# Performance work log

Measured on AMD Instinct MI355X. Metric: run time of the kernel, lower is better.

Reference implementation:

```python
import jax, jax.numpy as jnp
import numpy as np

B, T, M, D = 2, 2048, 2048, 128
H = M // D
ROTARY_BASE = 10000
NORM_EPS = 1e-6
QK_SCALE = 1.0 / D  # mult = sqrt(qk_scale) applied to both q and k
INFTY_APPROX = 1e30


def setup_inputs() -> dict:
    key = jax.random.key(0)
    ks = jax.random.split(key, 6)
    w_scale = M ** (-0.5)
    return {
        "x": jax.random.normal(ks[0], (B, T, M), jnp.float32),
        "wq": jax.random.normal(ks[1], (M, H, D), jnp.float32) * w_scale,
        "wk": jax.random.normal(ks[2], (M, H, D), jnp.float32) * w_scale,
        "wv": jax.random.normal(ks[3], (M, H, D), jnp.float32) * w_scale,
        "wo": jax.random.normal(ks[4], (H, D, M), jnp.float32) * w_scale,
        "gq": jnp.zeros((H, 1, D), jnp.float32),
        "bq": jnp.zeros((H, 1, D), jnp.float32),
        "gk": jnp.zeros((H, 1, D), jnp.float32),
        "bk": jnp.zeros((H, 1, D), jnp.float32),
    }


def _qk_layernorm(x, g, b):
    # x: [B,H,T,D]; g,b: [H,1,D]; centered RMS norm with trainable (1+g), b
    x = x - jnp.mean(x, axis=-1, keepdims=True)
    x = x / jnp.sqrt(jnp.mean(jnp.square(x), axis=-1, keepdims=True) + NORM_EPS)
    return x * (1.0 + g)[None] + b[None]


def _rotary(x):
    # x: [B,H,T,D]; half-split rotary encoding
    half = D // 2
    positions = jnp.arange(T, dtype=jnp.float32)[:, None]          # [T,1]
    ang_freqs = jnp.power(float(ROTARY_BASE), -jnp.arange(half, dtype=jnp.float32) / half)[None, :]  # [1,half]
    radians = positions * ang_freqs                                  # [T,half]
    cos = jnp.cos(radians)[None, None].astype(x.dtype)               # [1,1,T,half]
    sin = jnp.sin(radians)[None, None].astype(x.dtype)
    even, odd = jnp.split(x, 2, axis=-1)
    return jnp.concatenate([even * cos - odd * sin, even * sin + odd * cos], axis=-1)


def reference(x, wq, wk, wv, wo, gq, bq, gk, bk):
    q = jnp.einsum('bim,mhd->bhid', x, wq)
    k = jnp.einsum('bim,mhd->bhid', x, wk)
    v = jnp.einsum('bim,mhd->bhid', x, wv)
    q = _rotary(_qk_layernorm(q, gq, bq))
    k = _rotary(_qk_layernorm(k, gk, bk))
    mult = jnp.asarray(QK_SCALE ** 0.5, dtype=x.dtype)
    s = jnp.einsum('bhid,bhjd->bhij', q * mult, k * mult)            # [B,H,T,T]
    i = jnp.arange(T)[:, None]
    j = jnp.arange(T)[None, :]
    future = (i < j)[None, None]                                      # mask future positions
    s = s - jnp.asarray(INFTY_APPROX, dtype=s.dtype) * future
    p = jax.nn.softmax(s, axis=-1)
    o = jnp.einsum('bhij,bhjd->bhid', p, v)
    return jnp.einsum('bhid,hdm->bim', o, wo)
```

## Files before the change

### kernel.cpp

```cpp
#include <hip/hip_runtime.h>


#define NB 2
#define NT 2048
#define NM 2048
#define NH 16
#define ND 128

typedef __attribute__((ext_vector_type(4))) float f32x4;
typedef __attribute__((ext_vector_type(8))) short bf16x8;
typedef __attribute__((ext_vector_type(4))) short bf16x4;

#define AS1 __attribute__((address_space(1)))
#define AS3 __attribute__((address_space(3)))

__device__ __forceinline__ unsigned short f2bf(float f){
  unsigned int u = __float_as_uint(f);
  u = (u + 0x7fffu + ((u >> 16) & 1u)) >> 16;
  return (unsigned short)u;
}
__device__ __forceinline__ float bf2f(short s){
  return __uint_as_float(((unsigned int)(unsigned short)s) << 16);
}
__device__ __forceinline__ float wredsum(float v){
  #pragma unroll
  for (int m = 1; m < 64; m <<= 1) v += __shfl_xor(v, m);
  return v;
}
__device__ __forceinline__ void gload_lds16(const void* g, void* l){
  __builtin_amdgcn_global_load_lds((const AS1 void*)g, (AS3 void*)l, 16, 0, 0);
}

__global__ __launch_bounds__(64) void rope_table_k(float* ctab, float* stab){
  int t = blockIdx.x, i = threadIdx.x;
  float freq = __expf(-(float)i * (9.210340371976184f / 64.0f));
  float ang = (float)t * freq;
  ctab[t * 64 + i] = cosf(ang);
  stab[t * 64 + i] = sinf(ang);
}

__global__ __launch_bounds__(256) void cast_x_k(const float* __restrict__ x,
                                                short* __restrict__ xb){
  size_t gid = (size_t)blockIdx.x * 256 + threadIdx.x;
  float4 v = *(const float4*)(x + gid * 4);
  bf16x4 o;
  o[0] = (short)f2bf(v.x); o[1] = (short)f2bf(v.y);
  o[2] = (short)f2bf(v.z); o[3] = (short)f2bf(v.w);
  *(bf16x4*)(xb + gid * 4) = o;
}

__global__ __launch_bounds__(256) void transpose_w_k(const float* __restrict__ wq,
                                                     const float* __restrict__ wk,
                                                     const float* __restrict__ wv,
                                                     const float* __restrict__ wo,
                                                     short* __restrict__ wT){
  __shared__ float tl[32][33];
  int z = blockIdx.z;
  const float* src = (z == 0) ? wq : (z == 1) ? wk : (z == 2) ? wv : wo;
  short* dst = wT + (size_t)z * 2048 * 2048;
  int n0 = blockIdx.x * 32, k0 = blockIdx.y * 32;
  int cx = threadIdx.x & 31, ry = threadIdx.x >> 5;
  #pragma unroll
  for (int p = 0; p < 4; ++p)
    tl[ry + 8 * p][cx] = src[(size_t)(k0 + ry + 8 * p) * 2048 + n0 + cx];
  __syncthreads();
  #pragma unroll
  for (int p = 0; p < 4; ++p)
    dst[(size_t)(n0 + ry + 8 * p) * 2048 + k0 + cx] =
        (short)f2bf(tl[cx][ry + 8 * p]);
}

#define NKT 32
__global__ __launch_bounds__(512, 2) void gemm256_k(const short* __restrict__ A,
                                                    const short* __restrict__ Bt,
                                                    short* __restrict__ Cq){
  extern __shared__ char lds[];
  const int tid = threadIdx.x;
  const int wid = tid >> 6, lane = tid & 63;
  const int lrow = lane & 15, g8 = lane >> 4;
  const int wm = wid >> 2, wn = wid & 3;
  const int Kdim = 2048;

  int bid = blockIdx.x;
  int s = (bid & 7) * 48 + (bid >> 3);
  const int bx = s & 15;
  const int by = s >> 4;
  const int m0 = bx * 256, n0 = by * 256;

  const int r8 = lane >> 3;
  const int gcol = ((lane & 7) ^ r8) * 8;
  const short* Ab = A  + (size_t)(m0 + wid * 8 + r8) * Kdim + gcol;
  const short* Bb = Bt + (size_t)(n0 + wid * 8 + r8) * Kdim + gcol;

  f32x4 acc[8][4] = {};

  auto STAGE = [&](int c, int kt){
    #pragma unroll
    for (int h = 0; h < 2; ++h)
      #pragma unroll
      for (int l = 0; l < 2; ++l){
        size_t roff = (size_t)(h * 128 + l * 64) * Kdim + kt * 64;
        char* la = lds + c * 32768 + h * 16384 + l * 8192 + wid * 1024;
        gload_lds16(Ab + roff, la);
        gload_lds16(Bb + roff, la + 65536);
      }
  };
  auto ldA = [&](int c, int mi, int kk) -> bf16x8 {
    int row = mi * 16 + lrow;
    int col = (kk * 64 + g8 * 16) ^ ((lrow & 7) << 4);
    return *(const bf16x8*)(lds + c * 32768 + wm * 16384 + row * 128 + col);
  };
  auto ldB = [&](int c, int ni, int kk) -> bf16x8 {
    int row = (wn & 1) * 64 + ni * 16 + lrow;
    int col = (kk * 64 + g8 * 16) ^ ((lrow & 7) << 4);
    return *(const bf16x8*)(lds + 65536 + c * 32768 + (wn >> 1) * 16384 + row * 128 + col);
  };

  STAGE(0, 0);

  for (int kt = 0; kt < NKT; ++kt){
    const int c = kt & 1;
    asm volatile("s_waitcnt vmcnt(0)" ::: "memory");
    __builtin_amdgcn_s_barrier();
    if (kt + 1 < NKT) STAGE(c ^ 1, kt + 1);

    #pragma unroll
    for (int kk = 0; kk < 2; ++kk){
      bf16x8 bfr[4];
      #pragma unroll
      for (int ni = 0; ni < 4; ++ni) bfr[ni] = ldB(c, ni, kk);
      #pragma unroll
      for (int mh = 0; mh < 2; ++mh){
        bf16x8 afr[4];
        #pragma unroll
        for (int mi = 0; mi < 4; ++mi) afr[mi] = ldA(c, mh * 4 + mi, kk);
        #pragma unroll
        for (int mi = 0; mi < 4; ++mi)
          #pragma unroll
          for (int ni = 0; ni < 4; ++ni)
            acc[mh * 4 + mi][ni] = __builtin_amdgcn_mfma_f32_16x16x32_bf16(
                afr[mi], bfr[ni], acc[mh * 4 + mi][ni], 0, 0, 0);
      }
    }
  }

  #pragma unroll
  for (int mi = 0; mi < 8; ++mi){
    int rowb = m0 + wm * 128 + mi * 16 + g8 * 4;
    #pragma unroll
    for (int ni = 0; ni < 4; ++ni){
      int col = n0 + wn * 64 + ni * 16 + lrow;
      int tsel = col >> 11;
      int hd = col & 2047;
      int hh = hd >> 7, d = hd & 127;
      short* dst = Cq + (size_t)tsel * (NB * NH * NT * ND);
      f32x4 a = acc[mi][ni];
      #pragma unroll
      for (int r = 0; r < 4; ++r){
        int bt = rowb + r;
        int b = bt >> 11, t = bt & 2047;
        dst[(((size_t)(b * NH + hh)) * NT + t) * ND + d] = (short)f2bf(a[r]);
      }
    }
  }
}

__global__ __launch_bounds__(256) void gemm_bt_k(const short* __restrict__ A,
                                                 const short* __restrict__ Bt,
                                                 float* __restrict__ Cout,
                                                 int Kdim){
  __shared__ short As[2][128 * 32];
  __shared__ short Bs[2][128 * 32];
  const int tid = threadIdx.x;
  const int wid = tid >> 6, lane = tid & 63;
  const int lrow = lane & 15, g8 = lane >> 4;
  const int wm = wid >> 1, wn = wid & 1;
  const int m0 = blockIdx.x * 128, n0 = blockIdx.y * 128;
  f32x4 acc[4][4] = {};
  const int srow = lane >> 2;
  const int skcol = (lane & 3) * 8;

  auto STAGE = [&](int c, int kt){
    #pragma unroll
    for (int i = 0; i < 2; ++i){
      int inst = wid * 2 + i;
      int r = inst * 16 + srow;
      const short* sa = A  + (size_t)(m0 + r) * Kdim + kt + skcol;
      const short* sb = Bt + (size_t)(n0 + r) * Kdim + kt + skcol;
      gload_lds16(sa, (char*)As[c] + inst * 1024);
      gload_lds16(sb, (char*)Bs[c] + inst * 1024);
    }
  };

  STAGE(0, 0);
  const int nkt = Kdim >> 5;
  for (int it = 0; it < nkt; ++it){
    const int c = it & 1;
    asm volatile("s_waitcnt vmcnt(0)" ::: "memory");
    __builtin_amdgcn_s_barrier();
    if (it + 1 < nkt) STAGE(c ^ 1, (it + 1) << 5);

    bf16x8 af[4], bfv[4];
    #pragma unroll
    for (int mi = 0; mi < 4; ++mi)
      af[mi] = *(const bf16x8*)&As[c][(wm * 64 + mi * 16 + lrow) * 32 + g8 * 8];
    #pragma unroll
    for (int ni = 0; ni < 4; ++ni)
      bfv[ni] = *(const bf16x8*)&Bs[c][(wn * 64 + ni * 16 + lrow) * 32 + g8 * 8];
    #pragma unroll
    for (int mi = 0; mi < 4; ++mi)
      #pragma unroll
      for (int ni = 0; ni < 4; ++ni)
        acc[mi][ni] = __builtin_amdgcn_mfma_f32_16x16x32_bf16(
            af[mi], bfv[ni], acc[mi][ni], 0, 0, 0);
  }

  #pragma unroll
  for (int mi = 0; mi < 4; ++mi){
    int rowb = m0 + wm * 64 + mi * 16 + g8 * 4;
    #pragma unroll
    for (int ni = 0; ni < 4; ++ni){
      int col = n0 + wn * 64 + ni * 16 + lrow;
      f32x4 a = acc[mi][ni];
      #pragma unroll
      for (int r = 0; r < 4; ++r)
        Cout[(size_t)(rowb + r) * 2048 + col] = a[r];
    }
  }
}

__global__ __launch_bounds__(256) void norm_rope_k(const short* __restrict__ qkv,
                                                   short* __restrict__ outp,
                                                   const float* __restrict__ gq,
                                                   const float* __restrict__ bq,
                                                   const float* __restrict__ gk,
                                                   const float* __restrict__ bk,
                                                   const float* __restrict__ ctab,
                                                   const float* __restrict__ stab){
  int which = blockIdx.y;
  const short* src = qkv + (size_t)which * (NB * NH * NT * ND);
  short* dst = outp + (size_t)which * (NB * NH * NT * ND);
  const float* g = which ? gk : gq;
  const float* bb = which ? bk : bq;
  int wid = threadIdx.x >> 6, lane = threadIdx.x & 63;
  size_t row = (size_t)blockIdx.x * 4 + wid;
  int h = (int)((row >> 11) & 15);
  int t = (int)(row & 2047);
  const short* rp = src + row * ND;
  float v0 = bf2f(rp[lane]), v1 = bf2f(rp[lane + 64]);
  float mean = wredsum(v0 + v1) * (1.0f / 128.0f);
  float c0 = v0 - mean, c1 = v1 - mean;
  float ms = wredsum(c0 * c0 + c1 * c1) * (1.0f / 128.0f);
  float rstd = rsqrtf(ms + 1e-6f);
  float n0 = c0 * rstd * (1.0f + g[h * ND + lane]) + bb[h * ND + lane];
  float n1 = c1 * rstd * (1.0f + g[h * ND + lane + 64]) + bb[h * ND + lane + 64];
  float co = ctab[t * 64 + lane], si = stab[t * 64 + lane];
  short* wp = dst + row * ND;
  wp[lane]      = (short)f2bf(n0 * co - n1 * si);
  wp[lane + 64] = (short)f2bf(n0 * si + n1 * co);
}

__global__ __launch_bounds__(256) void attn_k(const short* __restrict__ qn,
                                              const short* __restrict__ kn,
                                              const short* __restrict__ vsrc,
                                              short* __restrict__ ob){
  __shared__ short Ks[64 * 128];
  __shared__ short VTs[128 * 64];
  __shared__ short Ps[4][16 * 64];
  const int tid = threadIdx.x;
  const int wid = tid >> 6, lane = tid & 63;
  const int lrow = lane & 15, g8 = lane >> 4;
  const int bh = blockIdx.y;
  const int b = bh >> 4, h = bh & 15;
  const size_t base = (size_t)bh * NT * ND;

  for (int pass = 0; pass < 2; ++pass){
    const int qt = pass ? (31 - (int)blockIdx.x) : (int)blockIdx.x;
    const int t0 = qt * 64;
    const int tq = t0 + wid * 16 + lrow;
    bf16x8 qf[4];
    #pragma unroll
    for (int dc = 0; dc < 4; ++dc)
      qf[dc] = *(const bf16x8*)(qn + base + (size_t)tq * ND + dc * 32 + g8 * 8);
    f32x4 O[8] = {};
    float m = -3e38f, lsum = 0.0f;
    const int ntiles = qt + 1;

    for (int jb = 0; jb < ntiles; ++jb){
      __syncthreads();
      #pragma unroll
      for (int p = 0; p < 4; ++p){
        int r = (tid >> 4) + p * 16;
        int c = tid & 15;
        bf16x8 kv = *(const bf16x8*)(kn + base + (size_t)(jb * 64 + r) * ND + c * 8);
        *(bf16x8*)((char*)Ks + r * 256 + ((c * 16) ^ ((r & 7) << 4))) = kv;
      }
      #pragma unroll
      for (int p = 0; p < 4; ++p){
        int jr = (tid >> 4) + p * 16;
        int d0 = (tid & 15) * 8;
        bf16x8 vv = *(const bf16x8*)(vsrc + base + (size_t)(jb * 64 + jr) * ND + d0);
        #pragma unroll
        for (int i = 0; i < 8; ++i){
          int d = d0 + i;
          *(short*)((char*)VTs + d * 128 +
                    ((jr * 2) ^ ((((d >> 3) ^ d) & 7) << 4))) = vv[i];
        }
      }
      __syncthreads();

      if (jb * 64 <= t0 + wid * 16 + 15){
        f32x4 st[4] = {};
        #pragma unroll
        for (int dc = 0; dc < 4; ++dc)
          #pragma unroll
          for (int js = 0; js < 4; ++js){
            int jl = js * 16 + lrow;
            bf16x8 kf = *(const bf16x8*)((char*)Ks + jl * 256 +
                          ((dc * 64 + g8 * 16) ^ ((jl & 7) << 4)));
            st[js] = __builtin_amdgcn_mfma_f32_16x16x32_bf16(kf, qf[dc], st[js], 0, 0, 0);
          }
        float mx = -3e38f;
        #pragma unroll
        for (int js = 0; js < 4; ++js)
          #pragma unroll
          for (int r = 0; r < 4; ++r){
            float s = st[js][r] * (1.0f / 128.0f);
            int j = jb * 64 + js * 16 + g8 * 4 + r;
            if (j > tq) s = -3e38f;
            st[js][r] = s;
            mx = fmaxf(mx, s);
          }
        mx = fmaxf(mx, __shfl_xor(mx, 16));
        mx = fmaxf(mx, __shfl_xor(mx, 32));
        float mnew = fmaxf(m, mx);
        float fac = __expf(m - mnew);
        m = mnew;
        lsum *= fac;
        #pragma unroll
        for (int dcb = 0; dcb < 8; ++dcb) O[dcb] *= fac;
        float ps = 0.0f;
        #pragma unroll
        for (int js = 0; js < 4; ++js)
          #pragma unroll
          for (int r = 0; r < 4; ++r){
            float p = __expf(st[js][r] - mnew);
            ps += p;
            int jl = js * 16 + g8 * 4 + r;
            *(short*)((char*)Ps[wid] + lrow * 128 +
                      ((jl * 2) ^ ((lrow & 7) << 4))) = (short)f2bf(p);
          }
        ps += __shfl_xor(ps, 16);
        ps += __shfl_xor(ps, 32);
        lsum += ps;
        asm volatile("s_waitcnt lgkmcnt(0)" ::: "memory");
        #pragma unroll
        for (int j32 = 0; j32 < 2; ++j32){
          bf16x8 pf = *(const bf16x8*)((char*)Ps[wid] + lrow * 128 +
                        ((j32 * 64 + g8 * 16) ^ ((lrow & 7) << 4)));
          #pragma unroll
          for (int dcb = 0; dcb < 8; ++dcb){
            int d = dcb * 16 + lrow;
            bf16x8 vf = *(const bf16x8*)((char*)VTs + d * 128 +
                          ((j32 * 64 + g8 * 16) ^ ((((d >> 3) ^ d) & 7) << 4)));
            O[dcb] = __builtin_amdgcn_mfma_f32_16x16x32_bf16(vf, pf, O[dcb], 0, 0, 0);
          }
        }
      }
    }
    float inv = 1.0f / lsum;
    #pragma unroll
    for (int dcb = 0; dcb < 8; ++dcb){
      bf16x4 w4;
      #pragma unroll
      for (int r = 0; r < 4; ++r) w4[r] = (short)f2bf(O[dcb][r] * inv);
      *(bf16x4*)(ob + ((size_t)(b * NT + tq)) * (NH * ND) + h * ND + dcb * 16 + g8 * 4) = w4;
    }
  }
}

extern "C" void kernel_launch(void* const* d_in, const int* in_sizes, int n_in,
                              void* d_out, int out_size, void* d_ws, size_t ws_size,
                              hipStream_t stream){
  const float* x  = (const float*)d_in[0];
  const float* wq = (const float*)d_in[1];
  const float* wk = (const float*)d_in[2];
  const float* wv = (const float*)d_in[3];
  const float* wo = (const float*)d_in[4];
  const float* gq = (const float*)d_in[5];
  const float* bq = (const float*)d_in[6];
  const float* gk = (const float*)d_in[7];
  const float* bk = (const float*)d_in[8];

  char* ws = (char*)d_ws;
  short* xb   = (short*)(ws);
  short* wT   = (short*)(ws + 16777216);
  short* qkvb = (short*)(ws + 50331648);
  short* qkn  = (short*)(ws + 100663296);
  short* ob   = (short*)(ws + 134217728);
  float* ctab = (float*)(ws + 150994944);
  float* stab = (float*)(ws + 151519232);

  (void)hipFuncSetAttribute((const void*)gemm256_k,
                            hipFuncAttributeMaxDynamicSharedMemorySize, 131072);

  rope_table_k<<<dim3(2048), dim3(64), 0, stream>>>(ctab, stab);
  cast_x_k<<<dim3(8192), dim3(256), 0, stream>>>(x, xb);
  transpose_w_k<<<dim3(64, 64, 4), dim3(256), 0, stream>>>(wq, wk, wv, wo, wT);
  gemm256_k<<<dim3(384), dim3(512), 131072, stream>>>(xb, wT, qkvb);
  norm_rope_k<<<dim3(16384, 2), dim3(256), 0, stream>>>(qkvb, qkn, gq, bq, gk, bk, ctab, stab);
  attn_k<<<dim3(16, 32), dim3(256), 0, stream>>>(qkn, qkn + 8388608,
                                                 qkvb + 2 * (size_t)8388608, ob);
  gemm_bt_k<<<dim3(32, 16), dim3(256), 0, stream>>>(ob, wT + 3 * (size_t)4194304,
                                                    (float*)d_out, 2048);
}
```

Before: 304.2 us.

## Store V transposed from QKV GEMM and double-buffer attention K/V tiles via direct global-to-LDS loads

The projection GEMM now writes V in a [b,h,d,t] transposed layout, so the attention kernel no longer has to transpose V element by element into shared memory. Attention K and V^T tiles are staged into swizzled double-buffered dynamic LDS with direct global-to-LDS loads, and the next tile is prefetched while the current one is computed. This replaces two full syncthreads per tile with a waitcnt plus barriers. The per-wave causal skip is dropped, so some fully masked subtiles are now computed, and LDS use per block rises to 72KB, which may lower occupancy.

```diff
diff --git a/kernel.cpp b/kernel.cpp
--- a/kernel.cpp
+++ b/kernel.cpp
@@ -155,11 +155,19 @@
       int hh = hd >> 7, d = hd & 127;
       short* dst = Cq + (size_t)tsel * (NB * NH * NT * ND);
       f32x4 a = acc[mi][ni];
-      #pragma unroll
-      for (int r = 0; r < 4; ++r){
-        int bt = rowb + r;
-        int b = bt >> 11, t = bt & 2047;
-        dst[(((size_t)(b * NH + hh)) * NT + t) * ND + d] = (short)f2bf(a[r]);
+      if (tsel == 2){
+        int b = rowb >> 11, t0 = rowb & 2047;
+        bf16x4 w4;
+        #pragma unroll
+        for (int r = 0; r < 4; ++r) w4[r] = (short)f2bf(a[r]);
+        *(bf16x4*)&dst[(((size_t)(b * NH + hh)) * ND + d) * NT + t0] = w4;
+      } else {
+        #pragma unroll
+        for (int r = 0; r < 4; ++r){
+          int bt = rowb + r;
+          int b = bt >> 11, t = bt & 2047;
+          dst[(((size_t)(b * NH + hh)) * NT + t) * ND + d] = (short)f2bf(a[r]);
+        }
       }
     }
   }
@@ -262,17 +270,35 @@
 
 __global__ __launch_bounds__(256) void attn_k(const short* __restrict__ qn,
                                               const short* __restrict__ kn,
-                                              const short* __restrict__ vsrc,
+                                              const short* __restrict__ vt,
                                               short* __restrict__ ob){
-  __shared__ short Ks[64 * 128];
-  __shared__ short VTs[128 * 64];
-  __shared__ short Ps[4][16 * 64];
+  extern __shared__ char lds[];
   const int tid = threadIdx.x;
   const int wid = tid >> 6, lane = tid & 63;
   const int lrow = lane & 15, g8 = lane >> 4;
   const int bh = blockIdx.y;
   const int b = bh >> 4, h = bh & 15;
   const size_t base = (size_t)bh * NT * ND;
+  char* Pw = lds + 65536 + wid * 2048;
+
+  auto STAGE = [&](int cb, int jb){
+    #pragma unroll
+    for (int i = 0; i < 4; ++i){
+      int r0 = wid * 16 + i * 4;
+      int r = r0 + (lane >> 4);
+      int g = lane & 15;
+      gload_lds16(kn + base + (size_t)(jb * 64 + r) * ND + ((g ^ (r & 7)) << 3),
+                  lds + cb * 16384 + r0 * 256);
+    }
+    #pragma unroll
+    for (int i = 0; i < 4; ++i){
+      int d0 = wid * 32 + i * 8;
+      int d = d0 + (lane >> 3);
+      int g = lane & 7;
+      gload_lds16(vt + base + (size_t)d * NT + jb * 64 + ((g ^ (d & 7)) << 3),
+                  lds + 32768 + cb * 16384 + d0 * 128);
+    }
+  };
 
   for (int pass = 0; pass < 2; ++pass){
     const int qt = pass ? (31 - (int)blockIdx.x) : (int)blockIdx.x;
@@ -286,87 +312,73 @@
     float m = -3e38f, lsum = 0.0f;
     const int ntiles = qt + 1;
 
+    __syncthreads();
+    STAGE(0, 0);
+
     for (int jb = 0; jb < ntiles; ++jb){
-      __syncthreads();
-      #pragma unroll
-      for (int p = 0; p < 4; ++p){
-        int r = (tid >> 4) + p * 16;
-        int c = tid & 15;
-        bf16x8 kv = *(const bf16x8*)(kn + base + (size_t)(jb * 64 + r) * ND + c * 8);
-        *(bf16x8*)((char*)Ks + r * 256 + ((c * 16) ^ ((r & 7) << 4))) = kv;
-      }
-      #pragma unroll
-      for (int p = 0; p < 4; ++p){
-        int jr = (tid >> 4) + p * 16;
-        int d0 = (tid & 15) * 8;
-        bf16x8 vv = *(const bf16x8*)(vsrc + base + (size_t)(jb * 64 + jr) * ND + d0);
-        #pragma unroll
-        for (int i = 0; i < 8; ++i){
-          int d = d0 + i;
-          *(short*)((char*)VTs + d * 128 +
-                    ((jr * 2) ^ ((((d >> 3) ^ d) & 7) << 4))) = vv[i];
+      const int cb = jb & 1;
+      asm volatile("s_waitcnt vmcnt(0)" ::: "memory");
+      __builtin_amdgcn_s_barrier();
+      if (jb + 1 < ntiles) STAGE(cb ^ 1, jb + 1);
+      const char* Kb = lds + cb * 16384;
+      const char* Vb = lds + 32768 + cb * 16384;
+
+      f32x4 st[4] = {};
+      #pragma unroll
+      for (int dc = 0; dc < 4; ++dc)
+        #pragma unroll
+        for (int js = 0; js < 4; ++js){
+          int jl = js * 16 + lrow;
+          bf16x8 kf = *(const bf16x8*)(Kb + jl * 256 +
+                        (((dc * 4 + g8) ^ (jl & 7)) << 4));
+          st[js] = __builtin_amdgcn_mfma_f32_16x16x32_bf16(kf, qf[dc], st[js], 0, 0, 0);
+        }
+      float mx = -3e38f;
+      #pragma unroll
+      for (int js = 0; js < 4; ++js)
+        #pragma unroll
+        for (int r = 0; r < 4; ++r){
+          float s = st[js][r] * (1.0f / 128.0f);
+          int j = jb * 64 + js * 16 + g8 * 4 + r;
+          if (j > tq) s = -3e38f;
+          st[js][r] = s;
+          mx = fmaxf(mx, s);
+        }
+      mx = fmaxf(mx, __shfl_xor(mx, 16));
+      mx = fmaxf(mx, __shfl_xor(mx, 32));
+      float mnew = fmaxf(m, mx);
+      float fac = __expf(m - mnew);
+      m = mnew;
+      lsum *= fac;
+      #pragma unroll
+      for (int dcb = 0; dcb < 8; ++dcb) O[dcb] *= fac;
+      float ps = 0.0f;
+      #pragma unroll
+      for (int js = 0; js < 4; ++js)
+        #pragma unroll
+        for (int r = 0; r < 4; ++r){
+          float p = __expf(st[js][r] - mnew);
+          ps += p;
+          int jl = js * 16 + g8 * 4 + r;
+          *(short*)(Pw + lrow * 128 + ((jl * 2) ^ ((lrow & 7) << 4))) = (short)f2bf(p);
+        }
+      ps += __shfl_xor(ps, 16);
+      ps += __shfl_xor(ps, 32);
+      lsum += ps;
+      asm volatile("s_waitcnt lgkmcnt(0)" ::: "memory");
+      #pragma unroll
+      for (int j32 = 0; j32 < 2; ++j32){
+        bf16x8 pf = *(const bf16x8*)(Pw + lrow * 128 +
+                      ((j32 * 64 + g8 * 16) ^ ((lrow & 7) << 4)));
+        #pragma unroll
+        for (int dcb = 0; dcb < 8; ++dcb){
+          int d = dcb * 16 + lrow;
+          bf16x8 vf = *(const bf16x8*)(Vb + d * 128 +
+                        (((j32 * 4 + g8) ^ (d & 7)) << 4));
+          O[dcb] = __builtin_amdgcn_mfma_f32_16x16x32_bf16(vf, pf, O[dcb], 0, 0, 0);
         }
       }
-      __syncthreads();
-
-      if (jb * 64 <= t0 + wid * 16 + 15){
-        f32x4 st[4] = {};
-        #pragma unroll
-        for (int dc = 0; dc < 4; ++dc)
-          #pragma unroll
-          for (int js = 0; js < 4; ++js){
-            int jl = js * 16 + lrow;
-            bf16x8 kf = *(const bf16x8*)((char*)Ks + jl * 256 +
-                          ((dc * 64 + g8 * 16) ^ ((jl & 7) << 4)));
-            st[js] = __builtin_amdgcn_mfma_f32_16x16x32_bf16(kf, qf[dc], st[js], 0, 0, 0);
-          }
-        float mx = -3e38f;
-        #pragma unroll
-        for (int js = 0; js < 4; ++js)
-          #pragma unroll
-          for (int r = 0; r < 4; ++r){
-            float s = st[js][r] * (1.0f / 128.0f);
-            int j = jb * 64 + js * 16 + g8 * 4 + r;
-            if (j > tq) s = -3e38f;
-            st[js][r] = s;
-            mx = fmaxf(mx, s);
-          }
-        mx = fmaxf(mx, __shfl_xor(mx, 16));
-        mx = fmaxf(mx, __shfl_xor(mx, 32));
-        float mnew = fmaxf(m, mx);
-        float fac = __expf(m - mnew);
-        m = mnew;
-        lsum *= fac;
-        #pragma unroll
-        for (int dcb = 0; dcb < 8; ++dcb) O[dcb] *= fac;
-        float ps = 0.0f;
-        #pragma unroll
-        for (int js = 0; js < 4; ++js)
-          #pragma unroll
-          for (int r = 0; r < 4; ++r){
-            float p = __expf(st[js][r] - mnew);
-            ps += p;
-            int jl = js * 16 + g8 * 4 + r;
-            *(short*)((char*)Ps[wid] + lrow * 128 +
-                      ((jl * 2) ^ ((lrow & 7) << 4))) = (short)f2bf(p);
-          }
-        ps += __shfl_xor(ps, 16);
-        ps += __shfl_xor(ps, 32);
-        lsum += ps;
-        asm volatile("s_waitcnt lgkmcnt(0)" ::: "memory");
-        #pragma unroll
-        for (int j32 = 0; j32 < 2; ++j32){
-          bf16x8 pf = *(const bf16x8*)((char*)Ps[wid] + lrow * 128 +
-                        ((j32 * 64 + g8 * 16) ^ ((lrow & 7) << 4)));
-          #pragma unroll
-          for (int dcb = 0; dcb < 8; ++dcb){
-            int d = dcb * 16 + lrow;
-            bf16x8 vf = *(const bf16x8*)((char*)VTs + d * 128 +
-                          ((j32 * 64 + g8 * 16) ^ ((((d >> 3) ^ d) & 7) << 4)));
-            O[dcb] = __builtin_amdgcn_mfma_f32_16x16x32_bf16(vf, pf, O[dcb], 0, 0, 0);
-          }
-        }
-      }
+      __builtin_amdgcn_s_barrier();
     }
     float inv = 1.0f / lsum;
     #pragma unroll
@@ -403,14 +415,16 @@
 
   (void)hipFuncSetAttribute((const void*)gemm256_k,
                             hipFuncAttributeMaxDynamicSharedMemorySize, 131072);
+  (void)hipFuncSetAttribute((const void*)attn_k,
+                            hipFuncAttributeMaxDynamicSharedMemorySize, 73728);
 
   rope_table_k<<<dim3(2048), dim3(64), 0, stream>>>(ctab, stab);
   cast_x_k<<<dim3(8192), dim3(256), 0, stream>>>(x, xb);
   transpose_w_k<<<dim3(64, 64, 4), dim3(256), 0, stream>>>(wq, wk, wv, wo, wT);
   gemm256_k<<<dim3(384), dim3(512), 131072, stream>>>(xb, wT, qkvb);
   norm_rope_k<<<dim3(16384, 2), dim3(256), 0, stream>>>(qkvb, qkn, gq, bq, gk, bk, ctab, stab);
-  attn_k<<<dim3(16, 32), dim3(256), 0, stream>>>(qkn, qkn + 8388608,
-                                                 qkvb + 2 * (size_t)8388608, ob);
+  attn_k<<<dim3(16, 32), dim3(256), 73728, stream>>>(qkn, qkn + 8388608,
+                                                     qkvb + 2 * (size_t)8388608, ob);
   gemm_bt_k<<<dim3(32, 16), dim3(256), 0, stream>>>(ob, wT + 3 * (size_t)4194304,
                                                     (float*)d_out, 2048);
 }
```

Measured after the change: 307.6 us. No clear change (+1.1%).
